# Kernel tuning notes

Measured on AMD Instinct MI355X. Metric: run time of the kernel, lower is better.

## Reference

```python
import jax, jax.numpy as jnp
import numpy as np

EPS = 1e-7
C = 1.0  # Poincare ball curvature

def _norm(v):
    return jnp.maximum(jnp.linalg.norm(v, axis=-1, keepdims=True), EPS)

def logmap0(x):
    n = _norm(x)
    n_c = jnp.minimum(n, 1.0 - 1e-5)
    return jnp.arctanh(jnp.sqrt(C) * n_c) * x / (jnp.sqrt(C) * n)

def expmap0(v):
    n = _norm(v)
    return jnp.tanh(jnp.sqrt(C) * n) * v / (jnp.sqrt(C) * n)

def hat_layer(x, W, a_src, a_dst, src, dst, num_nodes):
    # x: [N, in] on manifold; W: [in, H*D]; a_src/a_dst: [H, D]
    H, D = a_src.shape
    h = logmap0(x) @ W                       # tangent-space linear, [N, H*D]
    h = h.reshape(num_nodes, H, D)
    e_s = jnp.einsum('nhd,hd->nh', h, a_src)  # [N, H]
    e_d = jnp.einsum('nhd,hd->nh', h, a_dst)
    e = jax.nn.leaky_relu(e_s[src] + e_d[dst], 0.2)          # [E, H]
    emax = jax.ops.segment_max(e, dst, num_segments=num_nodes)
    emax = jnp.where(jnp.isfinite(emax), emax, 0.0)
    ee = jnp.exp(e - emax[dst])                               # [E, H]
    denom = jax.ops.segment_sum(ee, dst, num_segments=num_nodes)
    alpha = ee / (denom[dst] + 1e-16)                          # segment softmax
    msg = alpha[:, :, None] * h[src]                           # [E, H, D] (largest buffer)
    out = jax.ops.segment_sum(msg, dst, num_segments=num_nodes)
    return expmap0(out.reshape(num_nodes, H * D))

def setup_inputs() -> dict:
    key = jax.random.key(0)
    ks = jax.random.split(key, 9)
    N, E = 50000, 800000
    IN, HID, OUT, HEADS = 128, 64, 64, 4
    x = 0.05 * jax.random.normal(ks[0], (N, IN), dtype=jnp.float32)  # inside unit ball
    edge_index0 = jax.random.randint(ks[1], (2, E), 0, N, dtype=jnp.int32)
    edge_index1 = jax.random.randint(ks[2], (2, E), 0, N, dtype=jnp.int32)
    s = 0.05
    W1 = s * jax.random.normal(ks[3], (IN, HEADS * HID), dtype=jnp.float32)
    a_src1 = s * jax.random.normal(ks[4], (HEADS, HID), dtype=jnp.float32)
    a_dst1 = s * jax.random.normal(ks[5], (HEADS, HID), dtype=jnp.float32)
    W2 = s * jax.random.normal(ks[6], (HEADS * HID, OUT), dtype=jnp.float32)
    a_src2 = s * jax.random.normal(ks[7], (1, OUT), dtype=jnp.float32)
    a_dst2 = s * jax.random.normal(ks[8], (1, OUT), dtype=jnp.float32)
    return {"x": x, "W1": W1, "a_src1": a_src1, "a_dst1": a_dst1,
            "W2": W2, "a_src2": a_src2, "a_dst2": a_dst2,
            "edge_index0": edge_index0, "edge_index1": edge_index1}

def reference(x, W1, a_src1, a_dst1, W2, a_src2, a_dst2, edge_index0, edge_index1):
    N = x.shape[0]
    h = hat_layer(x, W1, a_src1, a_dst1, edge_index0[0], edge_index0[1], N)
    out = hat_layer(h, W2, a_src2, a_dst2, edge_index1[0], edge_index1[1], N)
    return out
```

## Files before the change

kernel.cpp:

```cpp
#include <hip/hip_runtime.h>

#define EPSF 1e-7f
#define NBMAX 512

typedef __attribute__((ext_vector_type(4))) _Float16 half4;
typedef __attribute__((ext_vector_type(8))) _Float16 half8;
typedef __attribute__((ext_vector_type(2))) _Float16 half2v;
typedef __attribute__((ext_vector_type(4))) float f32x4;
typedef unsigned long long u64;

__device__ __forceinline__ float lrelu02(float x){ return x > 0.f ? x : 0.2f*x; }

__global__ __launch_bounds__(256) void k_pre(
    const float* __restrict__ W1, const float* __restrict__ W2,
    const float* __restrict__ x,
    const int* __restrict__ dst0, int E0, const int* __restrict__ dst1, int E1,
    _Float16* __restrict__ w1t, _Float16* __restrict__ w2t,
    int* __restrict__ part0, int* __restrict__ part1,
    _Float16* __restrict__ lxh, int N) {
  const int b = blockIdx.x, tid = threadIdx.x;
  if (b < 128) {
    int idx = b*256 + tid;
    int j = idx >> 7, k = idx & 127;
    w1t[idx] = (_Float16)W1[(size_t)k*256 + j];
    return;
  }
  if (b < 192) {
    int idx = (b-128)*256 + tid;
    int j = idx >> 8, k = idx & 255;
    w2t[idx] = (_Float16)W2[(size_t)k*64 + j];
    return;
  }
  if (b < 704) {
    const int pb = b - 192;
    const int g = pb >> 8, p = pb & 255;
    const int* dst = g ? dst1 : dst0;
    const int E = g ? E1 : E0;
    int* part = g ? part1 : part0;
    __shared__ int hist[NBMAX];
    for (int i = tid; i < NBMAX; i += 256) hist[i] = 0;
    __syncthreads();
    const int per = (E + 255) >> 8;
    const int lo = p * per, hi = min(lo + per, E);
    for (int i = lo + tid; i < hi; i += 256)
      atomicAdd(&hist[dst[i] >> 7], 1);
    __syncthreads();
    for (int i = tid; i < NBMAX; i += 256) part[p*NBMAX + i] = hist[i];
    return;
  }
  int tidg = (b - 704)*256 + tid;
  int wid = tidg >> 6, lane = tidg & 63;
  int nw = (gridDim.x - 704) * 4;
  for (int row = wid; row < N; row += nw) {
    float2 v = *(const float2*)(x + (size_t)row*128 + lane*2);
    float ss = v.x*v.x + v.y*v.y;
    #pragma unroll
    for (int o = 32; o; o >>= 1) ss += __shfl_xor(ss, o);
    float n  = fmaxf(sqrtf(ss), EPSF);
    float nc = fminf(n, 1.f - 1e-5f);
    float sc = atanhf(nc) / n;
    half2v hv; hv.x = (_Float16)(v.x*sc); hv.y = (_Float16)(v.y*sc);
    *(half2v*)(lxh + (size_t)row*128 + lane*2) = hv;
  }
}

__global__ __launch_bounds__(256) void k_bucketA(
    const int* __restrict__ src0, const int* __restrict__ dst0,
    int* __restrict__ bcur0, u64* __restrict__ temp0, int E0, int blocksA0,
    const int* __restrict__ src1, const int* __restrict__ dst1,
    int* __restrict__ bcur1, u64* __restrict__ temp1, int E1, int nb) {
  const int g0 = (blockIdx.x < blocksA0);
  const int* src = g0 ? src0 : src1;
  const int* dst = g0 ? dst0 : dst1;
  int* bcur      = g0 ? bcur0 : bcur1;
  u64* temp      = g0 ? temp0 : temp1;
  const int E    = g0 ? E0 : E1;
  const int cb   = g0 ? blockIdx.x : blockIdx.x - blocksA0;
  __shared__ int hist[NBMAX];
  __shared__ int lbase[NBMAX];
  const int tid = threadIdx.x;
  const int chunk0 = cb * 4096;
  const int e_end = min(chunk0 + 4096, E);
  for (int i = tid; i < nb; i += 256) hist[i] = 0;
  __syncthreads();
  for (int i = chunk0 + tid; i < e_end; i += 256)
    atomicAdd(&hist[dst[i] >> 7], 1);
  __syncthreads();
  for (int bn = tid; bn < nb; bn += 256) {
    int c = hist[bn];
    lbase[bn] = c ? atomicAdd(&bcur[bn], c) : 0;
    hist[bn] = 0;
  }
  __syncthreads();
  for (int i = chunk0 + tid; i < e_end; i += 256) {
    int d = dst[i];
    int bn = d >> 7;
    int off = atomicAdd(&hist[bn], 1);
    temp[(size_t)lbase[bn] + off] = ((u64)(unsigned)d << 32) | (unsigned)src[i];
  }
}

__global__ __launch_bounds__(256) void k_bucketB2(
    const u64* __restrict__ temp0, const int* __restrict__ bbase0,
    int* __restrict__ rowptr0, int* __restrict__ csrc0,
    const float* __restrict__ es1, const float* __restrict__ ed1,
    half4* __restrict__ w0,
    const u64* __restrict__ temp1, const int* __restrict__ bbase1,
    int* __restrict__ rowptr1, int* __restrict__ csrc1, int N, int nb) {
  const int g0 = (blockIdx.x < nb);
  const u64* temp = g0 ? temp0 : temp1;
  const int* bbase = g0 ? bbase0 : bbase1;
  int* rowptr = g0 ? rowptr0 : rowptr1;
  int* csrc   = g0 ? csrc0 : csrc1;
  const int b = g0 ? blockIdx.x : blockIdx.x - nb;
  __shared__ int lcnt[128];
  __shared__ int lcur[128];
  __shared__ int wt4[4];
  __shared__ float ledv[512];
  const int tid = threadIdx.x;
  const int d0 = b << 7;
  const int d1 = min(d0 + 128, N);
  const int lo = bbase[b], hi = bbase[b+1];
  if (tid < 128) lcnt[tid] = 0;
  if (g0) {
    for (int i = tid; i < (d1 - d0)*4; i += 256) ledv[i] = ed1[d0*4 + i];
  }
  __syncthreads();
  for (int k = lo + tid; k < hi; k += 256)
    atomicAdd(&lcnt[(int)(temp[k] >> 32) - d0], 1);
  __syncthreads();
  int v = (tid < 128) ? lcnt[tid] : 0;
  const int lane = tid & 63, w = tid >> 6;
  int inc = v;
  #pragma unroll
  for (int o = 1; o < 64; o <<= 1) { int t = __shfl_up(inc, o); if (lane >= o) inc += t; }
  if (lane == 63) wt4[w] = inc;
  __syncthreads();
  int woff = 0;
  for (int i = 0; i < w; ++i) woff += wt4[i];
  int excl = lo + woff + inc - v;
  if (tid < d1 - d0) { rowptr[d0 + tid] = excl; lcur[tid] = excl; }
  if (b == nb-1 && tid == 0) rowptr[N] = hi;
  __syncthreads();
  for (int k = lo + tid; k < hi; k += 256) {
    u64 p = temp[k];
    int d = (int)(p >> 32);
    int s = (int)(unsigned)p;
    int pos = atomicAdd(&lcur[d - d0], 1);
    csrc[pos] = s;
    if (g0) {
      float4 e = *(const float4*)(es1 + (size_t)s*4);
      int ld = (d - d0)*4;
      half4 wh;
      wh.x = (_Float16)__expf(lrelu02(e.x + ledv[ld+0]));
      wh.y = (_Float16)__expf(lrelu02(e.y + ledv[ld+1]));
      wh.z = (_Float16)__expf(lrelu02(e.z + ledv[ld+2]));
      wh.w = (_Float16)__expf(lrelu02(e.w + ledv[ld+3]));
      w0[pos] = wh;
    }
  }
}

#define LXP 136
#define H1P 264
__global__ __launch_bounds__(256) void k_gemm1_mfma(
    const _Float16* __restrict__ lxh, const _Float16* __restrict__ w1t,
    const float* __restrict__ a_src, const float* __restrict__ a_dst,
    _Float16* __restrict__ h1h, float* __restrict__ es, float* __restrict__ ed,
    const int* __restrict__ part0, const int* __restrict__ part1,
    int* __restrict__ bbase0, int* __restrict__ bcur0,
    int* __restrict__ bbase1, int* __restrict__ bcur1, int nb, int N) {
  __shared__ _Float16 lxs[32*LXP];
  __shared__ _Float16 h1s[32*H1P];
  __shared__ int swt[4];
  const int tid = threadIdx.x;
  const int nblk = (N + 31) >> 5;
  if ((int)blockIdx.x >= nblk) {
    const int g = (int)blockIdx.x - nblk;
    const int* part = g ? part1 : part0;
    int* bbase = g ? bbase1 : bbase0;
    int* bcur  = g ? bcur1  : bcur0;
    const int i0 = tid*2, i1 = tid*2 + 1;
    int v0 = 0, v1 = 0;
    for (int p = 0; p < 256; ++p) {
      v0 += part[p*NBMAX + i0];
      v1 += part[p*NBMAX + i1];
    }
    int s = v0 + v1;
    const int lane = tid & 63, w = tid >> 6;
    int inc = s;
    #pragma unroll
    for (int o = 1; o < 64; o <<= 1) { int t = __shfl_up(inc, o); if (lane >= o) inc += t; }
    if (lane == 63) swt[w] = inc;
    __syncthreads();
    int woff = 0;
    for (int i = 0; i < w; ++i) woff += swt[i];
    int excl = woff + inc - s;
    if (i0 < nb) { bbase[i0] = excl; bcur[i0] = excl; }
    if (i1 < nb) { bbase[i1] = excl + v0; bcur[i1] = excl + v0; }
    if (tid == 255) bbase[nb] = excl + s;
    return;
  }
  const int block0 = blockIdx.x * 32;
  const int vrows = min(32, N - block0);
  for (int i = tid; i < 512; i += 256) {
    int r = i >> 4, c = (i & 15) * 8;
    uint4 v = make_uint4(0u,0u,0u,0u);
    if (r < vrows) v = *(const uint4*)(lxh + (size_t)(block0 + r)*128 + c);
    *(uint4*)(lxs + r*LXP + c) = v;
  }
  __syncthreads();
  const int wv = tid >> 6, lane = tid & 63;
  const int rt = wv & 1;
  const int ch = wv >> 1;
  const int arow = rt*16 + (lane & 15);
  const int koff = (lane >> 4) * 8;
  f32x4 acc[8];
  #pragma unroll
  for (int t = 0; t < 8; ++t) acc[t] = (f32x4){0.f,0.f,0.f,0.f};
  #pragma unroll
  for (int ks = 0; ks < 4; ++ks) {
    half8 a = *(const half8*)(lxs + arow*LXP + ks*32 + koff);
    #pragma unroll
    for (int t = 0; t < 8; ++t) {
      const int col0 = ch*128 + t*16;
      half8 b = *(const half8*)(w1t + (size_t)(col0 + (lane & 15))*128 + ks*32 + koff);
      acc[t] = __builtin_amdgcn_mfma_f32_16x16x32_f16(a, b, acc[t], 0, 0, 0);
    }
  }
  #pragma unroll
  for (int t = 0; t < 8; ++t) {
    const int col = ch*128 + t*16 + (lane & 15);
    #pragma unroll
    for (int r = 0; r < 4; ++r) {
      const int row = rt*16 + (lane >> 4)*4 + r;
      h1s[row*H1P + col] = (_Float16)acc[t][r];
    }
  }
  __syncthreads();
  for (int i = tid; i < 1024; i += 256) {
    int r = i >> 5, c = (i & 31) * 8;
    if (r < vrows) {
      uint4 v = *(const uint4*)(h1s + r*H1P + c);
      *(uint4*)(h1h + (size_t)(block0 + r)*256 + c) = v;
    }
  }
  const int head = lane >> 4;
  const float4 as4 = *(const float4*)(a_src + lane*4);
  const float4 ad4 = *(const float4*)(a_dst + lane*4);
  #pragma unroll
  for (int r8 = 0; r8 < 8; ++r8) {
    int rl = wv*8 + r8;
    int row = block0 + rl;
    if (row >= N) break;
    half4 hv = *(const half4*)(h1s + rl*H1P + lane*4);
    float ax = (float)hv.x, ay = (float)hv.y, az = (float)hv.z, aw = (float)hv.w;
    float ps = ax*as4.x + ay*as4.y + az*as4.z + aw*as4.w;
    float pd = ax*ad4.x + ay*ad4.y + az*ad4.z + aw*ad4.w;
    #pragma unroll
    for (int o = 8; o; o >>= 1) { ps += __shfl_xor(ps, o); pd += __shfl_xor(pd, o); }
    if ((lane & 15) == 0) { es[row*4 + head] = ps; ed[row*4 + head] = pd; }
  }
}

__global__ void k_agg1_csr(const int* __restrict__ rowptr, const int* __restrict__ csrc,
                           const half4* __restrict__ w0,
                           const _Float16* __restrict__ h1h, _Float16* __restrict__ t2h,
                           int N) {
  int tidg = blockIdx.x*blockDim.x + threadIdx.x;
  int wid = tidg >> 6, lane = tidg & 63;
  int nw = (gridDim.x * blockDim.x) >> 6;
  const int h = lane >> 4;
  const _Float16* wp = (const _Float16*)w0;
  half2v ones; ones.x = (_Float16)1.f; ones.y = (_Float16)1.f;
  for (int d = wid; d < N; d += nw) {
    const int beg = rowptr[d], end = rowptr[d+1];
    float4 acc = make_float4(0.f,0.f,0.f,0.f);
    float wsum = 0.f;
    int k = beg;
    const int kend4 = beg + ((end - beg) & ~3);
    if (k < kend4) {
      int s0 = csrc[k], s1 = csrc[k+1], s2 = csrc[k+2], s3 = csrc[k+3];
      half2v wab, wcd;
      wab.x = wp[(size_t)(k+0)*4 + h]; wab.y = wp[(size_t)(k+1)*4 + h];
      wcd.x = wp[(size_t)(k+2)*4 + h]; wcd.y = wp[(size_t)(k+3)*4 + h];
      for (;;) {
        half4 v0 = *(const half4*)(h1h + (size_t)s0*256 + lane*4);
        half4 v1 = *(const half4*)(h1h + (size_t)s1*256 + lane*4);
        half4 v2 = *(const half4*)(h1h + (size_t)s2*256 + lane*4);
        half4 v3 = *(const half4*)(h1h + (size_t)s3*256 + lane*4);
        k += 4;
        const bool more = (k < kend4);
        int t0 = 0, t1 = 0, t2 = 0, t3 = 0;
        half2v uab, ucd;
        uab.x = uab.y = ucd.x = ucd.y = (_Float16)0.f;
        if (more) {
          t0 = csrc[k]; t1 = csrc[k+1]; t2 = csrc[k+2]; t3 = csrc[k+3];
          uab.x = wp[(size_t)(k+0)*4 + h]; uab.y = wp[(size_t)(k+1)*4 + h];
          ucd.x = wp[(size_t)(k+2)*4 + h]; ucd.y = wp[(size_t)(k+3)*4 + h];
        }
        wsum = __builtin_amdgcn_fdot2(wab, ones, wsum, false);
        wsum = __builtin_amdgcn_fdot2(wcd, ones, wsum, false);
        half2v p;
        p.x = v0.x; p.y = v1.x;
        acc.x = __builtin_amdgcn_fdot2(p, wab, acc.x, false);
        p.x = v2.x; p.y = v3.x;
        acc.x = __builtin_amdgcn_fdot2(p, wcd, acc.x, false);
        p.x = v0.y; p.y = v1.y;
        acc.y = __builtin_amdgcn_fdot2(p, wab, acc.y, false);
        p.x = v2.y; p.y = v3.y;
        acc.y = __builtin_amdgcn_fdot2(p, wcd, acc.y, false);
        p.x = v0.z; p.y = v1.z;
        acc.z = __builtin_amdgcn_fdot2(p, wab, acc.z, false);
        p.x = v2.z; p.y = v3.z;
        acc.z = __builtin_amdgcn_fdot2(p, wcd, acc.z, false);
        p.x = v0.w; p.y = v1.w;
        acc.w = __builtin_amdgcn_fdot2(p, wab, acc.w, false);
        p.x = v2.w; p.y = v3.w;
        acc.w = __builtin_amdgcn_fdot2(p, wcd, acc.w, false);
        if (!more) break;
        s0 = t0; s1 = t1; s2 = t2; s3 = t3;
        wab = uab; wcd = ucd;
      }
    }
    for (; k < end; ++k) {
      int s = csrc[k];
      float wa = (float)wp[(size_t)k*4 + h];
      half4 hv = *(const half4*)(h1h + (size_t)s*256 + lane*4);
      wsum += wa;
      acc.x += wa*(float)hv.x; acc.y += wa*(float)hv.y;
      acc.z += wa*(float)hv.z; acc.w += wa*(float)hv.w;
    }
    float inv = 1.f / (wsum + 1e-16f);
    float ax = acc.x*inv, ay = acc.y*inv, az = acc.z*inv, aw = acc.w*inv;
    float ss = ax*ax + ay*ay + az*az + aw*aw;
    #pragma unroll
    for (int o = 32; o; o >>= 1) ss += __shfl_xor(ss, o);
    float n  = fmaxf(sqrtf(ss), EPSF);
    float s1 = tanhf(n) / n;
    float n2 = fmaxf(s1 * n, EPSF);
    float nc = fminf(n2, 1.f - 1e-5f);
    float sc = s1 * atanhf(nc) / n2;
    half4 o4; o4.x = (_Float16)(ax*sc); o4.y = (_Float16)(ay*sc);
              o4.z = (_Float16)(az*sc); o4.w = (_Float16)(aw*sc);
    *(half4*)(t2h + (size_t)d*256 + lane*4) = o4;
  }
}

#define T2SP 264
#define H2SP 72
__global__ __launch_bounds__(256) void k_gemm2_mfma(
    const _Float16* __restrict__ t2h, const _Float16* __restrict__ w2t,
    const float* __restrict__ a_src, const float* __restrict__ a_dst,
    _Float16* __restrict__ h2h, float* __restrict__ es, float* __restrict__ ed, int N) {
  __shared__ _Float16 t2s[32*T2SP];
  __shared__ _Float16 h2s[32*H2SP];
  const int tid = threadIdx.x;
  const int block0 = blockIdx.x * 32;
  const int vrows = min(32, N - block0);
  for (int i = tid; i < 1024; i += 256) {
    int r = i >> 5, c = (i & 31) * 8;
    uint4 v = make_uint4(0u,0u,0u,0u);
    if (r < vrows) v = *(const uint4*)(t2h + (size_t)(block0 + r)*256 + c);
    *(uint4*)(t2s + r*T2SP + c) = v;
  }
  __syncthreads();
  const int wv = tid >> 6, lane = tid & 63;
  const int rt = wv & 1;
  const int ch = wv >> 1;
  const int arow = rt*16 + (lane & 15);
  const int koff = (lane >> 4) * 8;
  f32x4 acc[2];
  acc[0] = (f32x4){0.f,0.f,0.f,0.f};
  acc[1] = (f32x4){0.f,0.f,0.f,0.f};
  #pragma unroll
  for (int ks = 0; ks < 8; ++ks) {
    half8 a = *(const half8*)(t2s + arow*T2SP + ks*32 + koff);
    #pragma unroll
    for (int t = 0; t < 2; ++t) {
      const int col0 = ch*32 + t*16;
      half8 b = *(const half8*)(w2t + (size_t)(col0 + (lane & 15))*256 + ks*32 + koff);
      acc[t] = __builtin_amdgcn_mfma_f32_16x16x32_f16(a, b, acc[t], 0, 0, 0);
    }
  }
  #pragma unroll
  for (int t = 0; t < 2; ++t) {
    const int col = ch*32 + t*16 + (lane & 15);
    #pragma unroll
    for (int r = 0; r < 4; ++r) {
      const int row = rt*16 + (lane >> 4)*4 + r;
      h2s[row*H2SP + col] = (_Float16)acc[t][r];
    }
  }
  __syncthreads();
  {
    int i = tid;
    int r = i >> 3, c = (i & 7) * 8;
    if (r < vrows) {
      uint4 v = *(const uint4*)(h2s + r*H2SP + c);
      *(uint4*)(h2h + (size_t)(block0 + r)*64 + c) = v;
    }
  }
  const int jj = (lane & 15) * 4;
  const int rg = lane >> 4;
  const int rbase = wv*8 + rg*2;
  const float4 as4 = *(const float4*)(a_src + jj);
  const float4 ad4 = *(const float4*)(a_dst + jj);
  #pragma unroll
  for (int rr = 0; rr < 2; ++rr) {
    int row = block0 + rbase + rr;
    if (row < N) {
      half4 hv = *(const half4*)(h2s + (rbase + rr)*H2SP + jj);
      float ax = (float)hv.x, ay = (float)hv.y, az = (float)hv.z, aw = (float)hv.w;
      float ps = ax*as4.x + ay*as4.y + az*as4.z + aw*as4.w;
      float pd = ax*ad4.x + ay*ad4.y + az*ad4.z + aw*ad4.w;
      #pragma unroll
      for (int o = 8; o; o >>= 1) { ps += __shfl_xor(ps, o); pd += __shfl_xor(pd, o); }
      if ((lane & 15) == 0) { es[row] = ps; ed[row] = pd; }
    }
  }
}

__global__ void k_agg2_csr(const int* __restrict__ rowptr, const int* __restrict__ csrc,
                           const float* __restrict__ es, const float* __restrict__ ed,
                           const _Float16* __restrict__ h2h, float* __restrict__ out, int N) {
  int tidg = blockIdx.x*blockDim.x + threadIdx.x;
  int wid = tidg >> 6, lane = tidg & 63;
  int nw = (gridDim.x * blockDim.x) >> 6;
  for (int d = wid; d < N; d += nw) {
    const int beg = rowptr[d], end = rowptr[d+1];
    const float edv = ed[d];
    float acc = 0.f, wsum = 0.f;
    int k = beg;
    const int kend4 = beg + ((end - beg) & ~3);
    if (k < kend4) {
      int s0 = csrc[k], s1 = csrc[k+1], s2 = csrc[k+2], s3 = csrc[k+3];
      for (;;) {
        float e0 = es[s0], e1 = es[s1], e2 = es[s2], e3 = es[s3];
        float x0 = (float)h2h[(size_t)s0*64 + lane];
        float x1 = (float)h2h[(size_t)s1*64 + lane];
        float x2 = (float)h2h[(size_t)s2*64 + lane];
        float x3 = (float)h2h[(size_t)s3*64 + lane];
        k += 4;
        const bool more = (k < kend4);
        int t0 = 0, t1 = 0, t2 = 0, t3 = 0;
        if (more) { t0 = csrc[k]; t1 = csrc[k+1]; t2 = csrc[k+2]; t3 = csrc[k+3]; }
        float w0 = __expf(lrelu02(e0 + edv));
        float w1 = __expf(lrelu02(e1 + edv));
        float w2 = __expf(lrelu02(e2 + edv));
        float w3 = __expf(lrelu02(e3 + edv));
        wsum += (w0 + w1) + (w2 + w3);
        acc += w0*x0 + w1*x1 + w2*x2 + w3*x3;
        if (!more) break;
        s0 = t0; s1 = t1; s2 = t2; s3 = t3;
      }
    }
    for (; k < end; ++k) {
      int s = csrc[k];
      float w = __expf(lrelu02(es[s] + edv));
      wsum += w;
      acc += w * (float)h2h[(size_t)s*64 + lane];
    }
    float a = acc / (wsum + 1e-16f);
    float ss = a*a;
    #pragma unroll
    for (int o = 32; o; o >>= 1) ss += __shfl_xor(ss, o);
    float n  = fmaxf(sqrtf(ss), EPSF);
    float sc = tanhf(n) / n;
    out[(size_t)d*64 + lane] = a * sc;
  }
}

extern "C" void kernel_launch(void* const* d_in, const int* in_sizes, int n_in,
                              void* d_out, int out_size, void* d_ws, size_t ws_size,
                              hipStream_t stream) {
  const float* x      = (const float*)d_in[0];
  const float* W1     = (const float*)d_in[1];
  const float* a_src1 = (const float*)d_in[2];
  const float* a_dst1 = (const float*)d_in[3];
  const float* W2     = (const float*)d_in[4];
  const float* a_src2 = (const float*)d_in[5];
  const float* a_dst2 = (const float*)d_in[6];
  const int*   ei0    = (const int*)d_in[7];
  const int*   ei1    = (const int*)d_in[8];
  const int N  = in_sizes[0] / 128;
  const int E0 = in_sizes[7] / 2;
  const int E1 = in_sizes[8] / 2;
  const int* src0 = ei0;  const int* dst0 = ei0 + E0;
  const int* src1 = ei1;  const int* dst1 = ei1 + E1;
  float* out = (float*)d_out;
  const int nb = (N + 127) >> 7;

  float* ws = (float*)d_ws;
  size_t o = 0;
  float* es1   = ws + o; o += (size_t)N*4;
  float* ed1   = ws + o; o += (size_t)N*4;
  float* es2   = ws + o; o += (size_t)N;
  float* ed2   = ws + o; o += (size_t)N;
  _Float16* lxh = (_Float16*)(ws + o); o += (size_t)N*64;
  _Float16* w1t = (_Float16*)(ws + o); o += 16384;
  _Float16* w2t = (_Float16*)(ws + o); o += 8192;
  _Float16* h1h = (_Float16*)(ws + o); o += (size_t)N*128;
  _Float16* t2h = (_Float16*)(ws + o); o += (size_t)N*128;
  _Float16* h2h = (_Float16*)(ws + o); o += (size_t)N*32;
  o += (o & 1);
  half4* w0    = (half4*)(ws + o); o += (size_t)E0*2;
  u64* temp0 = (u64*)(ws + o); o += (size_t)E0*2;
  u64* temp1 = (u64*)(ws + o); o += (size_t)E1*2;
  int* iws = (int*)(ws + o);
  size_t io = 0;
  int* rowptr0 = iws + io; io += N + 1;
  int* rowptr1 = iws + io; io += N + 1;
  int* part0   = iws + io; io += 256*NBMAX;
  int* part1   = iws + io; io += 256*NBMAX;
  int* bbase0  = iws + io; io += NBMAX + 1;
  int* bbase1  = iws + io; io += NBMAX + 1;
  int* bcur0   = iws + io; io += NBMAX;
  int* bcur1   = iws + io; io += NBMAX;
  int* csrc0   = iws + io; io += E0;
  int* csrc1   = iws + io; io += E1;

  dim3 blk(256);
  const int blocksA0 = (E0 + 4095) / 4096;
  const int blocksA1 = (E1 + 4095) / 4096;
  const int nblk1 = (N + 31) / 32;
  k_pre    <<<704 + 2048, blk, 0, stream>>>(W1, W2, x, dst0, E0, dst1, E1,
                                            w1t, w2t, part0, part1, lxh, N);
  k_gemm1_mfma<<<nblk1 + 2, blk, 0, stream>>>(lxh, w1t, a_src1, a_dst1,
                                              h1h, es1, ed1,
                                              part0, part1,
                                              bbase0, bcur0, bbase1, bcur1, nb, N);
  k_bucketA<<<blocksA0 + blocksA1, blk, 0, stream>>>(
      src0, dst0, bcur0, temp0, E0, blocksA0, src1, dst1, bcur1, temp1, E1, nb);
  k_bucketB2<<<2*nb, blk, 0, stream>>>(temp0, bbase0, rowptr0, csrc0,
                                       es1, ed1, w0,
                                       temp1, bbase1, rowptr1, csrc1, N, nb);
  k_agg1_csr<<<2048, blk, 0, stream>>>(rowptr0, csrc0, w0, h1h, t2h, N);
  k_gemm2_mfma<<<(N+31)/32, blk, 0, stream>>>(t2h, w2t, a_src2, a_dst2,
                                              h2h, es2, ed2, N);
  k_agg2_csr<<<2048, blk, 0, stream>>>(rowptr1, csrc1, es2, ed2, h2h, out, N);
}
```

Baseline: 229.3 us.

## Precompute layer-2 edge weights in a separate kernel and use fp16 dot2 accumulation

Layer-2 aggregation no longer computes exp(leaky_relu(es[src]+ed[dst])) per edge. A new kernel k_w1e precomputes the weights in fp16 into a CSR-ordered array, using a destination index array written by the bucketing kernel. The aggregation loop then reads the weights with software prefetch and accumulates with packed fp16 fdot2 instructions. In exchange it adds a kernel launch, extra global writes and reads (cdst1 and w1e), and some precision loss from fp16 weights and products.

```diff
diff --git a/kernel.cpp b/kernel.cpp
--- a/kernel.cpp
+++ b/kernel.cpp
@@ -106,7 +106,8 @@
     const float* __restrict__ es1, const float* __restrict__ ed1,
     half4* __restrict__ w0,
     const u64* __restrict__ temp1, const int* __restrict__ bbase1,
-    int* __restrict__ rowptr1, int* __restrict__ csrc1, int N, int nb) {
+    int* __restrict__ rowptr1, int* __restrict__ csrc1,
+    int* __restrict__ cdst1, int N, int nb) {
   const int g0 = (blockIdx.x < nb);
   const u64* temp = g0 ? temp0 : temp1;
   const int* bbase = g0 ? bbase0 : bbase1;
@@ -157,6 +158,8 @@
       wh.z = (_Float16)__expf(lrelu02(e.z + ledv[ld+2]));
       wh.w = (_Float16)__expf(lrelu02(e.w + ledv[ld+3]));
       w0[pos] = wh;
+    } else {
+      cdst1[pos] = d;
     }
   }
 }
@@ -421,45 +424,66 @@
   }
 }
 
+__global__ void k_w1e(const int* __restrict__ csrc, const int* __restrict__ cdst,
+                      const float* __restrict__ es, const float* __restrict__ ed,
+                      _Float16* __restrict__ w1e, int E) {
+  int i = blockIdx.x*blockDim.x + threadIdx.x;
+  int stride = gridDim.x*blockDim.x;
+  for (; i < E; i += stride) {
+    float e = es[csrc[i]] + ed[cdst[i]];
+    w1e[i] = (_Float16)__expf(lrelu02(e));
+  }
+}
+
 __global__ void k_agg2_csr(const int* __restrict__ rowptr, const int* __restrict__ csrc,
-                           const float* __restrict__ es, const float* __restrict__ ed,
+                           const _Float16* __restrict__ w1e,
                            const _Float16* __restrict__ h2h, float* __restrict__ out, int N) {
   int tidg = blockIdx.x*blockDim.x + threadIdx.x;
   int wid = tidg >> 6, lane = tidg & 63;
   int nw = (gridDim.x * blockDim.x) >> 6;
+  half2v ones; ones.x = (_Float16)1.f; ones.y = (_Float16)1.f;
   for (int d = wid; d < N; d += nw) {
     const int beg = rowptr[d], end = rowptr[d+1];
-    const float edv = ed[d];
     float acc = 0.f, wsum = 0.f;
     int k = beg;
     const int kend4 = beg + ((end - beg) & ~3);
     if (k < kend4) {
       int s0 = csrc[k], s1 = csrc[k+1], s2 = csrc[k+2], s3 = csrc[k+3];
+      half2v wab, wcd;
+      wab.x = w1e[k]; wab.y = w1e[k+1];
+      wcd.x = w1e[k+2]; wcd.y = w1e[k+3];
       for (;;) {
-        float e0 = es[s0], e1 = es[s1], e2 = es[s2], e3 = es[s3];
-        float x0 = (float)h2h[(size_t)s0*64 + lane];
-        float x1 = (float)h2h[(size_t)s1*64 + lane];
-        float x2 = (float)h2h[(size_t)s2*64 + lane];
-        float x3 = (float)h2h[(size_t)s3*64 + lane];
+        _Float16 x0 = h2h[(size_t)s0*64 + lane];
+        _Float16 x1 = h2h[(size_t)s1*64 + lane];
+        _Float16 x2 = h2h[(size_t)s2*64 + lane];
+        _Float16 x3 = h2h[(size_t)s3*64 + lane];
         k += 4;
         const bool more = (k < kend4);
         int t0 = 0, t1 = 0, t2 = 0, t3 = 0;
-        if (more) { t0 = csrc[k]; t1 = csrc[k+1]; t2 = csrc[k+2]; t3 = csrc[k+3]; }
-        float w0 = __expf(lrelu02(e0 + edv));
-        float w1 = __expf(lrelu02(e1 + edv));
-        float w2 = __expf(lrelu02(e2 + edv));
-        float w3 = __expf(lrelu02(e3 + edv));
-        wsum += (w0 + w1) + (w2 + w3);
-        acc += w0*x0 + w1*x1 + w2*x2 + w3*x3;
+        half2v uab, ucd;
+        uab.x = uab.y = ucd.x = ucd.y = (_Float16)0.f;
+        if (more) {
+          t0 = csrc[k]; t1 = csrc[k+1]; t2 = csrc[k+2]; t3 = csrc[k+3];
+          uab.x = w1e[k]; uab.y = w1e[k+1];
+          ucd.x = w1e[k+2]; ucd.y = w1e[k+3];
+        }
+        wsum = __builtin_amdgcn_fdot2(wab, ones, wsum, false);
+        wsum = __builtin_amdgcn_fdot2(wcd, ones, wsum, false);
+        half2v p;
+        p.x = x0; p.y = x1;
+        acc = __builtin_amdgcn_fdot2(p, wab, acc, false);
+        p.x = x2; p.y = x3;
+        acc = __builtin_amdgcn_fdot2(p, wcd, acc, false);
         if (!more) break;
         s0 = t0; s1 = t1; s2 = t2; s3 = t3;
+        wab = uab; wcd = ucd;
       }
     }
     for (; k < end; ++k) {
       int s = csrc[k];
-      float w = __expf(lrelu02(es[s] + edv));
-      wsum += w;
-      acc += w * (float)h2h[(size_t)s*64 + lane];
+      float wa = (float)w1e[k];
+      wsum += wa;
+      acc += wa * (float)h2h[(size_t)s*64 + lane];
     }
     float a = acc / (wsum + 1e-16f);
     float ss = a*a;
@@ -505,7 +529,8 @@
   _Float16* h2h = (_Float16*)(ws + o); o += (size_t)N*32;
   o += (o & 1);
   half4* w0    = (half4*)(ws + o); o += (size_t)E0*2;
-  u64* temp0 = (u64*)(ws + o); o += (size_t)E0*2;
+  _Float16* w1e = (_Float16*)(ws + o); o += (size_t)(E1+1)/2;
+  u64* temp0 = (u64*)(ws + o); o += (o & 1), o += (size_t)E0*2;
   u64* temp1 = (u64*)(ws + o); o += (size_t)E1*2;
   int* iws = (int*)(ws + o);
   size_t io = 0;
@@ -519,6 +544,7 @@
   int* bcur1   = iws + io; io += NBMAX;
   int* csrc0   = iws + io; io += E0;
   int* csrc1   = iws + io; io += E1;
+  int* cdst1   = iws + io; io += E1;
 
   dim3 blk(256);
   const int blocksA0 = (E0 + 4095) / 4096;
@@ -534,9 +560,10 @@
       src0, dst0, bcur0, temp0, E0, blocksA0, src1, dst1, bcur1, temp1, E1, nb);
   k_bucketB2<<<2*nb, blk, 0, stream>>>(temp0, bbase0, rowptr0, csrc0,
                                        es1, ed1, w0,
-                                       temp1, bbase1, rowptr1, csrc1, N, nb);
+                                       temp1, bbase1, rowptr1, csrc1, cdst1, N, nb);
   k_agg1_csr<<<2048, blk, 0, stream>>>(rowptr0, csrc0, w0, h1h, t2h, N);
   k_gemm2_mfma<<<(N+31)/32, blk, 0, stream>>>(t2h, w2t, a_src2, a_dst2,
                                               h2h, es2, ed2, N);
-  k_agg2_csr<<<2048, blk, 0, stream>>>(rowptr1, csrc1, es2, ed2, h2h, out, N);
-}
+  k_w1e    <<<1024, blk, 0, stream>>>(csrc1, cdst1, es2, ed2, w1e, E1);
+  k_agg2_csr<<<2048, blk, 0, stream>>>(rowptr1, csrc1, w1e, h2h, out, N);
+}
```

Measured after the change: 232.8 us. About the same (+1.5%).
